# Kernel optimization log

Hardware: AMD Instinct MI355X
Metric: run time of the kernel (lower is better)

## Reference

```python
import jax, jax.numpy as jnp
import numpy as np

B, G, CIN, COUT, K = 4, 32768, 64, 64, 3
FM = (256, 256)  # fm_shape -> grid_size = 1/FM
SIG_CLIP = 9.21  # safe_sigmoid: sigmoid of clipped logits


def setup_inputs() -> dict:
    key = jax.random.key(0)
    k1, k2, k3 = jax.random.split(key, 3)
    instance_feature = jax.random.normal(k1, (B, G, CIN), dtype=jnp.float32)
    anchor = jax.random.normal(k2, (B, G, 2), dtype=jnp.float32)
    weight = jax.random.normal(k3, (K, K, CIN, COUT), dtype=jnp.float32) * 0.05
    return {"instance_feature": instance_feature, "anchor": anchor, "weight": weight}


def reference(instance_feature, anchor, weight):
    b, g = instance_feature.shape[:2]
    H, W = FM
    grid_size = 1.0 / jnp.array(FM, dtype=jnp.float32)

    # ---- index construction (matches torch forward) ----
    anchor_xy = jax.nn.sigmoid(jnp.clip(anchor[..., :2], -SIG_CLIP, SIG_CLIP)).reshape(-1, 2)
    idx = ((anchor_xy - anchor_xy.min(axis=0, keepdims=True)) / grid_size).astype(jnp.int32)  # [N,2], in [0,FM)
    batch_ids = jnp.repeat(jnp.arange(b, dtype=jnp.int32), g)  # [N]

    feats = instance_feature.reshape(b * g, -1).astype(jnp.float32)  # [N,Cin]
    N = feats.shape[0]

    # ---- submanifold conv: dense (b,H,W) voxel -> point-id map (rulebook) ----
    grid = jnp.full((b, H, W), -1, dtype=jnp.int32)
    grid = grid.at[batch_ids, idx[:, 0], idx[:, 1]].max(jnp.arange(N, dtype=jnp.int32))

    pad = (K - 1) // 2
    out = jnp.zeros((N, weight.shape[-1]), dtype=jnp.float32)
    for dy in range(K):
        for dx in range(K):
            ny = idx[:, 0] + (dy - pad)
            nx = idx[:, 1] + (dx - pad)
            inb = (ny >= 0) & (ny < H) & (nx >= 0) & (nx < W)
            nid = grid[batch_ids, jnp.clip(ny, 0, H - 1), jnp.clip(nx, 0, W - 1)]  # [N]
            valid = inb & (nid >= 0)
            nfeat = jnp.where(valid[:, None], feats[jnp.maximum(nid, 0)], 0.0)  # gather
            out = out + nfeat @ weight[dy, dx]  # GEMM + accumulate (scatter is identity for SubM)
    return out.reshape(b, g, -1)  # out_proj is Identity (use_out_proj=False)
```

## Files before the change

### kernel.cpp

```cpp
#include <hip/hip_runtime.h>

#define NPTS  131072
#define GPTS  32768

typedef __attribute__((ext_vector_type(4)))  _Float16 half4v;
typedef __attribute__((ext_vector_type(8)))  _Float16 half8v;
typedef __attribute__((ext_vector_type(16))) float    f32x16;

__device__ __forceinline__ float sigf(float x) {
    x = fminf(fmaxf(x, -9.21f), 9.21f);
    float t = (float)exp(-(double)x);
    return 1.0f / (1.0f + t);
}

__global__ __launch_bounds__(256) void k_front(const float* __restrict__ anchor,
                                               const float* __restrict__ W,
                                               const float* __restrict__ feats,
                                               float* __restrict__ s0a,
                                               float* __restrict__ s1a,
                                               float2* __restrict__ blockmin,
                                               _Float16* __restrict__ bpk,
                                               _Float16* __restrict__ fb,
                                               int* __restrict__ grd) {
    const int bid = blockIdx.x;
    if (bid < 512) {
        __shared__ float red[8];
        int i = bid * 256 + threadIdx.x;
        int2 mone = {-1, -1};
        ((int2*)grd)[i] = mone;
        float2 a = ((const float2*)anchor)[i];
        float s0 = sigf(a.x);
        float s1 = sigf(a.y);
        s0a[i] = s0;
        s1a[i] = s1;
        float m0 = s0, m1 = s1;
        #pragma unroll
        for (int off = 32; off; off >>= 1) {
            m0 = fminf(m0, __shfl_down(m0, off));
            m1 = fminf(m1, __shfl_down(m1, off));
        }
        int wv = threadIdx.x >> 6;
        if ((threadIdx.x & 63) == 0) { red[wv * 2] = m0; red[wv * 2 + 1] = m1; }
        __syncthreads();
        if (threadIdx.x == 0) {
            float a0 = fminf(fminf(red[0], red[2]), fminf(red[4], red[6]));
            float a1 = fminf(fminf(red[1], red[3]), fminf(red[5], red[7]));
            blockmin[bid] = make_float2(a0, a1);
        }
    } else if (bid < 530) {
        int tid = (bid - 512) * 256 + threadIdx.x;
        if (tid >= 4608) return;
        int l  = tid & 63;
        int q  = tid >> 6;
        int nt = q & 1;
        int ks = (q >> 1) & 3;
        int t  = q >> 3;
        int n  = nt * 32 + (l & 31);
        int kb = ks * 16 + (l >> 5) * 8;
        half8v v;
        #pragma unroll
        for (int j = 0; j < 8; ++j)
            v[j] = (_Float16)W[(t * 64 + kb + j) * 64 + n];
        ((half8v*)bpk)[q * 64 + l] = v;
    } else {
        int tid = (bid - 530) * 256 + threadIdx.x;
        if (bid == 530 && threadIdx.x < 8) {
            half8v z = {};
            *(half8v*)(fb + (long)NPTS * 64 + threadIdx.x * 8) = z;
        }
        #pragma unroll
        for (int r = 0; r < 4; ++r) {
            long i = tid + (long)r * 524288;
            float4 f = ((const float4*)feats)[i];
            half4v o = {(_Float16)f.x, (_Float16)f.y, (_Float16)f.z, (_Float16)f.w};
            *(half4v*)(fb + i * 4) = o;
        }
    }
}

__global__ __launch_bounds__(256) void k_grid(const float* __restrict__ s0a,
                                              const float* __restrict__ s1a,
                                              const float2* __restrict__ blockmin,
                                              int* __restrict__ pidx,
                                              int* __restrict__ grid) {
    __shared__ float red[8];
    float2 ba = blockmin[threadIdx.x];
    float2 bb = blockmin[threadIdx.x + 256];
    float m0 = fminf(ba.x, bb.x), m1 = fminf(ba.y, bb.y);
    #pragma unroll
    for (int off = 32; off; off >>= 1) {
        m0 = fminf(m0, __shfl_down(m0, off));
        m1 = fminf(m1, __shfl_down(m1, off));
    }
    int wv = threadIdx.x >> 6;
    if ((threadIdx.x & 63) == 0) { red[wv * 2] = m0; red[wv * 2 + 1] = m1; }
    __syncthreads();
    m0 = fminf(fminf(red[0], red[2]), fminf(red[4], red[6]));
    m1 = fminf(fminf(red[1], red[3]), fminf(red[5], red[7]));

    int i = blockIdx.x * 256 + threadIdx.x;
    int iy = (int)((s0a[i] - m0) * 256.0f);
    int ix = (int)((s1a[i] - m1) * 256.0f);
    pidx[i] = (iy << 8) | ix;
    int b = i >> 15;
    atomicMax(&grid[(b << 16) + (iy << 8) + ix], i);
}

__global__ __launch_bounds__(256, 4) void k_mconv(const _Float16* __restrict__ fb,
                                                  const _Float16* __restrict__ bpk,
                                                  const int* __restrict__ pidx,
                                                  const int* __restrict__ grid,
                                                  float* __restrict__ out) {
    const int lane  = threadIdx.x & 63;
    const int wv    = threadIdx.x >> 6;
    const int pbase = (blockIdx.x << 7) + (wv << 5);
    const int prow  = lane & 31;
    const int khalf = lane >> 5;
    const int p     = pbase + prow;

    const int pk = pidx[p];
    const int iy = pk >> 8;
    const int ix = pk & 255;
    const int* gb = grid + ((p >> 15) << 16);

    int nid[9];
    #pragma unroll
    for (int t = 0; t < 9; ++t) {
        const int ny = iy + t / 3 - 1;
        const int nx = ix + t % 3 - 1;
        int n = ((unsigned)ny < 256u && (unsigned)nx < 256u) ? gb[(ny << 8) + nx] : -1;
        nid[t] = (n < 0) ? NPTS : n;
    }

    const half8v* bq = (const half8v*)bpk + lane;

    f32x16 acc0, acc1;
    #pragma unroll
    for (int r = 0; r < 16; ++r) { acc0[r] = 0.0f; acc1[r] = 0.0f; }

    #pragma unroll
    for (int t = 0; t < 9; ++t) {
        const half8v* arow = (const half8v*)(fb + ((long)nid[t] << 6));
        half8v a0 = arow[khalf];
        half8v a1 = arow[2 + khalf];
        half8v a2 = arow[4 + khalf];
        half8v a3 = arow[6 + khalf];
        const half8v* bt = bq + (t << 9);
        acc0 = __builtin_amdgcn_mfma_f32_32x32x16_f16(a0, bt[0 * 64], acc0, 0, 0, 0);
        acc1 = __builtin_amdgcn_mfma_f32_32x32x16_f16(a0, bt[1 * 64], acc1, 0, 0, 0);
        acc0 = __builtin_amdgcn_mfma_f32_32x32x16_f16(a1, bt[2 * 64], acc0, 0, 0, 0);
        acc1 = __builtin_amdgcn_mfma_f32_32x32x16_f16(a1, bt[3 * 64], acc1, 0, 0, 0);
        acc0 = __builtin_amdgcn_mfma_f32_32x32x16_f16(a2, bt[4 * 64], acc0, 0, 0, 0);
        acc1 = __builtin_amdgcn_mfma_f32_32x32x16_f16(a2, bt[5 * 64], acc1, 0, 0, 0);
        acc0 = __builtin_amdgcn_mfma_f32_32x32x16_f16(a3, bt[6 * 64], acc0, 0, 0, 0);
        acc1 = __builtin_amdgcn_mfma_f32_32x32x16_f16(a3, bt[7 * 64], acc1, 0, 0, 0);
    }

    #pragma unroll
    for (int r = 0; r < 16; ++r) {
        int orow = pbase + (r & 3) + ((r >> 2) << 3) + (khalf << 2);
        out[(long)orow * 64 + prow]      = acc0[r];
        out[(long)orow * 64 + 32 + prow] = acc1[r];
    }
}

extern "C" void kernel_launch(void* const* d_in, const int* in_sizes, int n_in,
                              void* d_out, int out_size, void* d_ws, size_t ws_size,
                              hipStream_t stream) {
    const float* inst   = (const float*)d_in[0];
    const float* anchor = (const float*)d_in[1];
    const float* W      = (const float*)d_in[2];
    float* out = (float*)d_out;

    char* ws = (char*)d_ws;
    float*     s0a  = (float*)(ws);
    float*     s1a  = (float*)(ws + 524288);
    int*       pidx = (int*)(ws + 1048576);
    int*       grd  = (int*)(ws + 1572864);
    float2*    bmin = (float2*)(ws + 2621440);
    _Float16*  fb   = (_Float16*)(ws + 2625536);
    _Float16*  bpk  = (_Float16*)(ws + 19402880);

    k_front<<<2578, 256, 0, stream>>>(anchor, W, inst, s0a, s1a, bmin, bpk, fb, grd);
    k_grid <<<512,  256, 0, stream>>>(s0a, s1a, bmin, pidx, grd);
    k_mconv<<<1024, 256, 0, stream>>>(fb, bpk, pidx, grd, out);
}
```

Baseline: 55.40 us.

## Materialize dense per-cell fp16 feature grid to remove indirect neighbor lookups

Replaces the per-point fp16 feature buffer with a dense per-voxel fp16 buffer filled by a new kernel that reads the grid's winning point id for every cell. The conv kernel then addresses neighbor rows directly by cell index, dropping the dependent grid load before each feature gather. The cost is a 262144-row dense buffer (twice the point count) that must be written in full, including zero rows for empty cells, plus one extra kernel launch.

```diff
diff --git a/kernel.cpp b/kernel.cpp
--- a/kernel.cpp
+++ b/kernel.cpp
@@ -2,8 +2,9 @@
 
 #define NPTS  131072
 #define GPTS  32768
-
-typedef __attribute__((ext_vector_type(4)))  _Float16 half4v;
+#define NCELL 262144
+#define ZROW  262144
+
 typedef __attribute__((ext_vector_type(8)))  _Float16 half8v;
 typedef __attribute__((ext_vector_type(16))) float    f32x16;
 
@@ -15,12 +16,10 @@
 
 __global__ __launch_bounds__(256) void k_front(const float* __restrict__ anchor,
                                                const float* __restrict__ W,
-                                               const float* __restrict__ feats,
                                                float* __restrict__ s0a,
                                                float* __restrict__ s1a,
                                                float2* __restrict__ blockmin,
                                                _Float16* __restrict__ bpk,
-                                               _Float16* __restrict__ fb,
                                                int* __restrict__ grd) {
     const int bid = blockIdx.x;
     if (bid < 512) {
@@ -47,7 +46,7 @@
             float a1 = fminf(fminf(red[1], red[3]), fminf(red[5], red[7]));
             blockmin[bid] = make_float2(a0, a1);
         }
-    } else if (bid < 530) {
+    } else {
         int tid = (bid - 512) * 256 + threadIdx.x;
         if (tid >= 4608) return;
         int l  = tid & 63;
@@ -62,19 +61,6 @@
         for (int j = 0; j < 8; ++j)
             v[j] = (_Float16)W[(t * 64 + kb + j) * 64 + n];
         ((half8v*)bpk)[q * 64 + l] = v;
-    } else {
-        int tid = (bid - 530) * 256 + threadIdx.x;
-        if (bid == 530 && threadIdx.x < 8) {
-            half8v z = {};
-            *(half8v*)(fb + (long)NPTS * 64 + threadIdx.x * 8) = z;
-        }
-        #pragma unroll
-        for (int r = 0; r < 4; ++r) {
-            long i = tid + (long)r * 524288;
-            float4 f = ((const float4*)feats)[i];
-            half4v o = {(_Float16)f.x, (_Float16)f.y, (_Float16)f.z, (_Float16)f.w};
-            *(half4v*)(fb + i * 4) = o;
-        }
     }
 }
 
@@ -106,10 +92,38 @@
     atomicMax(&grid[(b << 16) + (iy << 8) + ix], i);
 }
 
-__global__ __launch_bounds__(256, 4) void k_mconv(const _Float16* __restrict__ fb,
+__global__ __launch_bounds__(256) void k_fill(const float* __restrict__ feats,
+                                              const int* __restrict__ grd,
+                                              _Float16* __restrict__ cfb) {
+    int c = blockIdx.x * 256 + threadIdx.x;
+    int nid = grd[c];
+    _Float16* dst = cfb + ((long)c << 6);
+    if (nid >= 0) {
+        const float4* src = (const float4*)(feats + ((long)nid << 6));
+        #pragma unroll
+        for (int q = 0; q < 8; ++q) {
+            float4 f = src[2 * q];
+            float4 g = src[2 * q + 1];
+            half8v o = {(_Float16)f.x, (_Float16)f.y, (_Float16)f.z, (_Float16)f.w,
+                        (_Float16)g.x, (_Float16)g.y, (_Float16)g.z, (_Float16)g.w};
+            ((half8v*)dst)[q] = o;
+        }
+    } else {
+        half8v z = {};
+        #pragma unroll
+        for (int q = 0; q < 8; ++q) ((half8v*)dst)[q] = z;
+    }
+    if (c == 0) {
+        half8v z = {};
+        _Float16* zr = cfb + ((long)ZROW << 6);
+        #pragma unroll
+        for (int q = 0; q < 8; ++q) ((half8v*)zr)[q] = z;
+    }
+}
+
+__global__ __launch_bounds__(256, 4) void k_mconv(const _Float16* __restrict__ cfb,
                                                   const _Float16* __restrict__ bpk,
                                                   const int* __restrict__ pidx,
-                                                  const int* __restrict__ grid,
                                                   float* __restrict__ out) {
     const int lane  = threadIdx.x & 63;
     const int wv    = threadIdx.x >> 6;
@@ -121,15 +135,15 @@
     const int pk = pidx[p];
     const int iy = pk >> 8;
     const int ix = pk & 255;
-    const int* gb = grid + ((p >> 15) << 16);
-
-    int nid[9];
+    const int bbase = (p >> 15) << 16;
+
+    int row[9];
     #pragma unroll
     for (int t = 0; t < 9; ++t) {
         const int ny = iy + t / 3 - 1;
         const int nx = ix + t % 3 - 1;
-        int n = ((unsigned)ny < 256u && (unsigned)nx < 256u) ? gb[(ny << 8) + nx] : -1;
-        nid[t] = (n < 0) ? NPTS : n;
+        row[t] = ((unsigned)ny < 256u && (unsigned)nx < 256u)
+                   ? bbase + (ny << 8) + nx : ZROW;
     }
 
     const half8v* bq = (const half8v*)bpk + lane;
@@ -140,7 +154,7 @@
 
     #pragma unroll
     for (int t = 0; t < 9; ++t) {
-        const half8v* arow = (const half8v*)(fb + ((long)nid[t] << 6));
+        const half8v* arow = (const half8v*)(cfb + ((long)row[t] << 6));
         half8v a0 = arow[khalf];
         half8v a1 = arow[2 + khalf];
         half8v a2 = arow[4 + khalf];
@@ -178,10 +192,11 @@
     int*       pidx = (int*)(ws + 1048576);
     int*       grd  = (int*)(ws + 1572864);
     float2*    bmin = (float2*)(ws + 2621440);
-    _Float16*  fb   = (_Float16*)(ws + 2625536);
-    _Float16*  bpk  = (_Float16*)(ws + 19402880);
-
-    k_front<<<2578, 256, 0, stream>>>(anchor, W, inst, s0a, s1a, bmin, bpk, fb, grd);
+    _Float16*  bpk  = (_Float16*)(ws + 2625536);
+    _Float16*  cfb  = (_Float16*)(ws + 2703360);
+
+    k_front<<<530,  256, 0, stream>>>(anchor, W, s0a, s1a, bmin, bpk, grd);
     k_grid <<<512,  256, 0, stream>>>(s0a, s1a, bmin, pidx, grd);
-    k_mconv<<<1024, 256, 0, stream>>>(fb, bpk, pidx, grd, out);
-}
+    k_fill <<<1024, 256, 0, stream>>>(inst, grd, cfb);
+    k_mconv<<<1024, 256, 0, stream>>>(cfb, bpk, pidx, out);
+}
```

After: 71.59 us. +29.2%, slower.

## Bin points into spatial 16x16 tiles and stage halo features in LDS

Applied to the files above, without the earlier changes.

Points are bucketed by 16x16 grid tile using a histogram, a single-block scan and a scatter. Each conv block then loads the 18x18 halo of neighbour features into swizzled shared memory once and runs the MFMA GEMMs from LDS. This replaces repeated global gathers of neighbour rows. The cost is two extra kernel launches, atomics, a serial single-block scan, uneven tile occupancy and lower occupancy from the 41KB LDS buffer.

```diff
diff --git a/kernel.cpp b/kernel.cpp
--- a/kernel.cpp
+++ b/kernel.cpp
@@ -21,13 +21,15 @@
                                                float2* __restrict__ blockmin,
                                                _Float16* __restrict__ bpk,
                                                _Float16* __restrict__ fb,
-                                               int* __restrict__ grd) {
+                                               int* __restrict__ grd,
+                                               int* __restrict__ thist) {
     const int bid = blockIdx.x;
     if (bid < 512) {
         __shared__ float red[8];
         int i = bid * 256 + threadIdx.x;
         int2 mone = {-1, -1};
         ((int2*)grd)[i] = mone;
+        if (i < 1024) thist[i] = 0;
         float2 a = ((const float2*)anchor)[i];
         float s0 = sigf(a.x);
         float s1 = sigf(a.y);
@@ -64,10 +66,6 @@
         ((half8v*)bpk)[q * 64 + l] = v;
     } else {
         int tid = (bid - 530) * 256 + threadIdx.x;
-        if (bid == 530 && threadIdx.x < 8) {
-            half8v z = {};
-            *(half8v*)(fb + (long)NPTS * 64 + threadIdx.x * 8) = z;
-        }
         #pragma unroll
         for (int r = 0; r < 4; ++r) {
             long i = tid + (long)r * 524288;
@@ -82,7 +80,8 @@
                                               const float* __restrict__ s1a,
                                               const float2* __restrict__ blockmin,
                                               int* __restrict__ pidx,
-                                              int* __restrict__ grid) {
+                                              int* __restrict__ grid,
+                                              int* __restrict__ thist) {
     __shared__ float red[8];
     float2 ba = blockmin[threadIdx.x];
     float2 bb = blockmin[threadIdx.x + 256];
@@ -104,63 +103,129 @@
     pidx[i] = (iy << 8) | ix;
     int b = i >> 15;
     atomicMax(&grid[(b << 16) + (iy << 8) + ix], i);
-}
-
-__global__ __launch_bounds__(256, 4) void k_mconv(const _Float16* __restrict__ fb,
+    int tile = (b << 8) | ((iy >> 4) << 4) | (ix >> 4);
+    atomicAdd(&thist[tile], 1);
+}
+
+__global__ __launch_bounds__(256) void k_scan(const int* __restrict__ thist,
+                                              int* __restrict__ tstart,
+                                              int* __restrict__ tcur) {
+    __shared__ int sd[256];
+    int tid = threadIdx.x;
+    int4 h = ((const int4*)thist)[tid];
+    int s = h.x + h.y + h.z + h.w;
+    sd[tid] = s;
+    __syncthreads();
+    #pragma unroll
+    for (int off = 1; off < 256; off <<= 1) {
+        int v = (tid >= off) ? sd[tid - off] : 0;
+        __syncthreads();
+        sd[tid] += v;
+        __syncthreads();
+    }
+    int excl = sd[tid] - s;
+    int4 o;
+    o.x = excl; o.y = o.x + h.x; o.z = o.y + h.y; o.w = o.z + h.z;
+    ((int4*)tstart)[tid] = o;
+    ((int4*)tcur)[tid]   = o;
+    if (tid == 255) tstart[1024] = sd[255];
+}
+
+__global__ __launch_bounds__(256) void k_tscat(const int* __restrict__ pidx,
+                                               int* __restrict__ tcur,
+                                               int* __restrict__ tlist) {
+    int i = blockIdx.x * 256 + threadIdx.x;
+    int pk = pidx[i];
+    int iy = pk >> 8, ix = pk & 255;
+    int b = i >> 15;
+    int tile = (b << 8) | ((iy >> 4) << 4) | (ix >> 4);
+    int slot = atomicAdd(&tcur[tile], 1);
+    tlist[slot] = i | ((iy & 15) << 17) | ((ix & 15) << 21);
+}
+
+__global__ __launch_bounds__(256, 3) void k_mconv(const _Float16* __restrict__ fb,
                                                   const _Float16* __restrict__ bpk,
-                                                  const int* __restrict__ pidx,
                                                   const int* __restrict__ grid,
+                                                  const int* __restrict__ tstart,
+                                                  const int* __restrict__ tlist,
                                                   float* __restrict__ out) {
+    __shared__ half8v bsh[2592];
+
+    const int bid = blockIdx.x;
+    const int b  = bid >> 8;
+    const int ty = (bid >> 4) & 15;
+    const int tx = bid & 15;
+
+    for (int s = threadIdx.x; s < 324; s += 256) {
+        int hy = (ty << 4) - 1 + s / 18;
+        int hx = (tx << 4) - 1 + s % 18;
+        int nid = -1;
+        if ((unsigned)hy < 256u && (unsigned)hx < 256u)
+            nid = grid[(b << 16) + (hy << 8) + hx];
+        half8v* dst = &bsh[s * 8];
+        int sw = s & 7;
+        if (nid >= 0) {
+            const half8v* src = (const half8v*)(fb + ((long)nid << 6));
+            #pragma unroll
+            for (int q = 0; q < 8; ++q) dst[q ^ sw] = src[q];
+        } else {
+            half8v z = {};
+            #pragma unroll
+            for (int q = 0; q < 8; ++q) dst[q] = z;
+        }
+    }
+
+    const int tb = tstart[bid];
+    const int np = tstart[bid + 1] - tb;
+    __syncthreads();
+    if (np == 0) return;
+
     const int lane  = threadIdx.x & 63;
     const int wv    = threadIdx.x >> 6;
-    const int pbase = (blockIdx.x << 7) + (wv << 5);
     const int prow  = lane & 31;
     const int khalf = lane >> 5;
-    const int p     = pbase + prow;
-
-    const int pk = pidx[p];
-    const int iy = pk >> 8;
-    const int ix = pk & 255;
-    const int* gb = grid + ((p >> 15) << 16);
-
-    int nid[9];
-    #pragma unroll
-    for (int t = 0; t < 9; ++t) {
-        const int ny = iy + t / 3 - 1;
-        const int nx = ix + t % 3 - 1;
-        int n = ((unsigned)ny < 256u && (unsigned)nx < 256u) ? gb[(ny << 8) + nx] : -1;
-        nid[t] = (n < 0) ? NPTS : n;
-    }
-
     const half8v* bq = (const half8v*)bpk + lane;
 
-    f32x16 acc0, acc1;
-    #pragma unroll
-    for (int r = 0; r < 16; ++r) { acc0[r] = 0.0f; acc1[r] = 0.0f; }
-
-    #pragma unroll
-    for (int t = 0; t < 9; ++t) {
-        const half8v* arow = (const half8v*)(fb + ((long)nid[t] << 6));
-        half8v a0 = arow[khalf];
-        half8v a1 = arow[2 + khalf];
-        half8v a2 = arow[4 + khalf];
-        half8v a3 = arow[6 + khalf];
-        const half8v* bt = bq + (t << 9);
-        acc0 = __builtin_amdgcn_mfma_f32_32x32x16_f16(a0, bt[0 * 64], acc0, 0, 0, 0);
-        acc1 = __builtin_amdgcn_mfma_f32_32x32x16_f16(a0, bt[1 * 64], acc1, 0, 0, 0);
-        acc0 = __builtin_amdgcn_mfma_f32_32x32x16_f16(a1, bt[2 * 64], acc0, 0, 0, 0);
-        acc1 = __builtin_amdgcn_mfma_f32_32x32x16_f16(a1, bt[3 * 64], acc1, 0, 0, 0);
-        acc0 = __builtin_amdgcn_mfma_f32_32x32x16_f16(a2, bt[4 * 64], acc0, 0, 0, 0);
-        acc1 = __builtin_amdgcn_mfma_f32_32x32x16_f16(a2, bt[5 * 64], acc1, 0, 0, 0);
-        acc0 = __builtin_amdgcn_mfma_f32_32x32x16_f16(a3, bt[6 * 64], acc0, 0, 0, 0);
-        acc1 = __builtin_amdgcn_mfma_f32_32x32x16_f16(a3, bt[7 * 64], acc1, 0, 0, 0);
-    }
-
-    #pragma unroll
-    for (int r = 0; r < 16; ++r) {
-        int orow = pbase + (r & 3) + ((r >> 2) << 3) + (khalf << 2);
-        out[(long)orow * 64 + prow]      = acc0[r];
-        out[(long)orow * 64 + 32 + prow] = acc1[r];
+    for (int base = wv * 32; base < np; base += 128) {
+        const int npw = np - base;
+        const int myi = base + prow;
+        const int e = tlist[tb + ((myi < np) ? myi : np - 1)];
+        const int ly = ((e >> 17) & 15) + 1;
+        const int lx = ((e >> 21) & 15) + 1;
+
+        f32x16 acc0, acc1;
+        #pragma unroll
+        for (int r = 0; r < 16; ++r) { acc0[r] = 0.0f; acc1[r] = 0.0f; }
+
+        #pragma unroll
+        for (int t = 0; t < 9; ++t) {
+            const int r  = (ly + t / 3 - 1) * 18 + (lx + t % 3 - 1);
+            const int rb = r * 8;
+            const int sw = r & 7;
+            half8v a0 = bsh[rb + ((0 + khalf) ^ sw)];
+            half8v a1 = bsh[rb + ((2 + khalf) ^ sw)];
+            half8v a2 = bsh[rb + ((4 + khalf) ^ sw)];
+            half8v a3 = bsh[rb + ((6 + khalf) ^ sw)];
+            const half8v* bt = bq + (t << 9);
+            acc0 = __builtin_amdgcn_mfma_f32_32x32x16_f16(a0, bt[0 * 64], acc0, 0, 0, 0);
+            acc1 = __builtin_amdgcn_mfma_f32_32x32x16_f16(a0, bt[1 * 64], acc1, 0, 0, 0);
+            acc0 = __builtin_amdgcn_mfma_f32_32x32x16_f16(a1, bt[2 * 64], acc0, 0, 0, 0);
+            acc1 = __builtin_amdgcn_mfma_f32_32x32x16_f16(a1, bt[3 * 64], acc1, 0, 0, 0);
+            acc0 = __builtin_amdgcn_mfma_f32_32x32x16_f16(a2, bt[4 * 64], acc0, 0, 0, 0);
+            acc1 = __builtin_amdgcn_mfma_f32_32x32x16_f16(a2, bt[5 * 64], acc1, 0, 0, 0);
+            acc0 = __builtin_amdgcn_mfma_f32_32x32x16_f16(a3, bt[6 * 64], acc0, 0, 0, 0);
+            acc1 = __builtin_amdgcn_mfma_f32_32x32x16_f16(a3, bt[7 * 64], acc1, 0, 0, 0);
+        }
+
+        #pragma unroll
+        for (int r = 0; r < 16; ++r) {
+            int pr = (r & 3) + ((r >> 2) << 3) + (khalf << 2);
+            if (pr < npw) {
+                int op = tlist[tb + base + pr] & 0x1FFFF;
+                out[(long)op * 64 + prow]      = acc0[r];
+                out[(long)op * 64 + 32 + prow] = acc1[r];
+            }
+        }
     }
 }
 
@@ -173,15 +238,21 @@
     float* out = (float*)d_out;
 
     char* ws = (char*)d_ws;
-    float*     s0a  = (float*)(ws);
-    float*     s1a  = (float*)(ws + 524288);
-    int*       pidx = (int*)(ws + 1048576);
-    int*       grd  = (int*)(ws + 1572864);
-    float2*    bmin = (float2*)(ws + 2621440);
-    _Float16*  fb   = (_Float16*)(ws + 2625536);
-    _Float16*  bpk  = (_Float16*)(ws + 19402880);
-
-    k_front<<<2578, 256, 0, stream>>>(anchor, W, inst, s0a, s1a, bmin, bpk, fb, grd);
-    k_grid <<<512,  256, 0, stream>>>(s0a, s1a, bmin, pidx, grd);
-    k_mconv<<<1024, 256, 0, stream>>>(fb, bpk, pidx, grd, out);
-}
+    float*     s0a    = (float*)(ws);
+    float*     s1a    = (float*)(ws + 524288);
+    int*       pidx   = (int*)(ws + 1048576);
+    int*       grd    = (int*)(ws + 1572864);
+    float2*    bmin   = (float2*)(ws + 2621440);
+    int*       thist  = (int*)(ws + 2625536);
+    int*       tstart = (int*)(ws + 2629632);
+    int*       tcur   = (int*)(ws + 2637824);
+    int*       tlist  = (int*)(ws + 2641920);
+    _Float16*  fb     = (_Float16*)(ws + 3166208);
+    _Float16*  bpk    = (_Float16*)(ws + 19943424);
+
+    k_front<<<2578, 256, 0, stream>>>(anchor, W, inst, s0a, s1a, bmin, bpk, fb, grd, thist);
+    k_grid <<<512,  256, 0, stream>>>(s0a, s1a, bmin, pidx, grd, thist);
+    k_scan <<<1,    256, 0, stream>>>(thist, tstart, tcur);
+    k_tscat<<<512,  256, 0, stream>>>(pidx, tcur, tlist);
+    k_mconv<<<1024, 256, 0, stream>>>(fb, bpk, grd, tstart, tlist, out);
+}
```

After: 205.4 us. 271% more time.

## Split 3x3 taps across wave pairs with LDS reduction in mconv

Applied to the files above, without the earlier changes.

Each 32-point tile is now handled by two waves: one computes taps 0-4 and the other taps 5-8. The second wave's partial accumulators are summed in via shared memory before the store. The grid doubles to 2048 blocks and launch bounds rise to 6 blocks per CU. The aim is more parallelism and a shorter serial gather-to-MFMA chain per wave, paid for with a 16KB LDS buffer, a barrier and duplicated index lookups.

```diff
diff --git a/kernel.cpp b/kernel.cpp
--- a/kernel.cpp
+++ b/kernel.cpp
@@ -106,14 +106,18 @@
     atomicMax(&grid[(b << 16) + (iy << 8) + ix], i);
 }
 
-__global__ __launch_bounds__(256, 4) void k_mconv(const _Float16* __restrict__ fb,
+__global__ __launch_bounds__(256, 6) void k_mconv(const _Float16* __restrict__ fb,
                                                   const _Float16* __restrict__ bpk,
                                                   const int* __restrict__ pidx,
                                                   const int* __restrict__ grid,
                                                   float* __restrict__ out) {
+    __shared__ float lred[2][32][64];
+
     const int lane  = threadIdx.x & 63;
     const int wv    = threadIdx.x >> 6;
-    const int pbase = (blockIdx.x << 7) + (wv << 5);
+    const int half  = wv & 1;
+    const int tile  = wv >> 1;
+    const int pbase = (blockIdx.x << 6) + (tile << 5);
     const int prow  = lane & 31;
     const int khalf = lane >> 5;
     const int p     = pbase + prow;
@@ -123,13 +127,21 @@
     const int ix = pk & 255;
     const int* gb = grid + ((p >> 15) << 16);
 
-    int nid[9];
-    #pragma unroll
-    for (int t = 0; t < 9; ++t) {
-        const int ny = iy + t / 3 - 1;
-        const int nx = ix + t % 3 - 1;
-        int n = ((unsigned)ny < 256u && (unsigned)nx < 256u) ? gb[(ny << 8) + nx] : -1;
-        nid[t] = (n < 0) ? NPTS : n;
+    const int t0 = half ? 5 : 0;
+    const int nt = half ? 4 : 5;
+
+    int nid[5];
+    #pragma unroll
+    for (int u = 0; u < 5; ++u) {
+        if (u < nt) {
+            const int t  = t0 + u;
+            const int ny = iy + t / 3 - 1;
+            const int nx = ix + t % 3 - 1;
+            int n = ((unsigned)ny < 256u && (unsigned)nx < 256u) ? gb[(ny << 8) + nx] : -1;
+            nid[u] = (n < 0) ? NPTS : n;
+        } else {
+            nid[u] = NPTS;
+        }
     }
 
     const half8v* bq = (const half8v*)bpk + lane;
@@ -139,28 +151,43 @@
     for (int r = 0; r < 16; ++r) { acc0[r] = 0.0f; acc1[r] = 0.0f; }
 
     #pragma unroll
-    for (int t = 0; t < 9; ++t) {
-        const half8v* arow = (const half8v*)(fb + ((long)nid[t] << 6));
-        half8v a0 = arow[khalf];
-        half8v a1 = arow[2 + khalf];
-        half8v a2 = arow[4 + khalf];
-        half8v a3 = arow[6 + khalf];
-        const half8v* bt = bq + (t << 9);
-        acc0 = __builtin_amdgcn_mfma_f32_32x32x16_f16(a0, bt[0 * 64], acc0, 0, 0, 0);
-        acc1 = __builtin_amdgcn_mfma_f32_32x32x16_f16(a0, bt[1 * 64], acc1, 0, 0, 0);
-        acc0 = __builtin_amdgcn_mfma_f32_32x32x16_f16(a1, bt[2 * 64], acc0, 0, 0, 0);
-        acc1 = __builtin_amdgcn_mfma_f32_32x32x16_f16(a1, bt[3 * 64], acc1, 0, 0, 0);
-        acc0 = __builtin_amdgcn_mfma_f32_32x32x16_f16(a2, bt[4 * 64], acc0, 0, 0, 0);
-        acc1 = __builtin_amdgcn_mfma_f32_32x32x16_f16(a2, bt[5 * 64], acc1, 0, 0, 0);
-        acc0 = __builtin_amdgcn_mfma_f32_32x32x16_f16(a3, bt[6 * 64], acc0, 0, 0, 0);
-        acc1 = __builtin_amdgcn_mfma_f32_32x32x16_f16(a3, bt[7 * 64], acc1, 0, 0, 0);
-    }
-
-    #pragma unroll
-    for (int r = 0; r < 16; ++r) {
-        int orow = pbase + (r & 3) + ((r >> 2) << 3) + (khalf << 2);
-        out[(long)orow * 64 + prow]      = acc0[r];
-        out[(long)orow * 64 + 32 + prow] = acc1[r];
+    for (int u = 0; u < 5; ++u) {
+        if (u < nt) {
+            const int t = t0 + u;
+            const half8v* arow = (const half8v*)(fb + ((long)nid[u] << 6));
+            half8v a0 = arow[khalf];
+            half8v a1 = arow[2 + khalf];
+            half8v a2 = arow[4 + khalf];
+            half8v a3 = arow[6 + khalf];
+            const half8v* bt = bq + (t << 9);
+            acc0 = __builtin_amdgcn_mfma_f32_32x32x16_f16(a0, bt[0 * 64], acc0, 0, 0, 0);
+            acc1 = __builtin_amdgcn_mfma_f32_32x32x16_f16(a0, bt[1 * 64], acc1, 0, 0, 0);
+            acc0 = __builtin_amdgcn_mfma_f32_32x32x16_f16(a1, bt[2 * 64], acc0, 0, 0, 0);
+            acc1 = __builtin_amdgcn_mfma_f32_32x32x16_f16(a1, bt[3 * 64], acc1, 0, 0, 0);
+            acc0 = __builtin_amdgcn_mfma_f32_32x32x16_f16(a2, bt[4 * 64], acc0, 0, 0, 0);
+            acc1 = __builtin_amdgcn_mfma_f32_32x32x16_f16(a2, bt[5 * 64], acc1, 0, 0, 0);
+            acc0 = __builtin_amdgcn_mfma_f32_32x32x16_f16(a3, bt[6 * 64], acc0, 0, 0, 0);
+            acc1 = __builtin_amdgcn_mfma_f32_32x32x16_f16(a3, bt[7 * 64], acc1, 0, 0, 0);
+        }
+    }
+
+    if (half) {
+        #pragma unroll
+        for (int r = 0; r < 16; ++r) {
+            lred[tile][r][lane]      = acc0[r];
+            lred[tile][16 + r][lane] = acc1[r];
+        }
+    }
+    __syncthreads();
+    if (!half) {
+        #pragma unroll
+        for (int r = 0; r < 16; ++r) {
+            float v0 = acc0[r] + lred[tile][r][lane];
+            float v1 = acc1[r] + lred[tile][16 + r][lane];
+            int orow = pbase + (r & 3) + ((r >> 2) << 3) + (khalf << 2);
+            out[(long)orow * 64 + prow]      = v0;
+            out[(long)orow * 64 + 32 + prow] = v1;
+        }
     }
 }
 
@@ -183,5 +210,5 @@
 
     k_front<<<2578, 256, 0, stream>>>(anchor, W, inst, s0a, s1a, bmin, bpk, fb, grd);
     k_grid <<<512,  256, 0, stream>>>(s0a, s1a, bmin, pidx, grd);
-    k_mconv<<<1024, 256, 0, stream>>>(fb, bpk, pidx, grd, out);
-}
+    k_mconv<<<2048, 256, 0, stream>>>(fb, bpk, pidx, grd, out);
+}
```

Result: no change. 55.72 us (+0.6%).
